# Kernel tuning notes

Measured on AMD Instinct MI355X. Metric: run time of the kernel, lower is better.

Reference implementation:

```python
import jax, jax.numpy as jnp
import numpy as np

N_FIELDS = 8
N_NODES = 100000
N_EDGES = 6400000


def setup_inputs() -> dict:
    key = jax.random.key(0)
    k1, k2, k3, k4, k5 = jax.random.split(key, 5)
    q = jax.random.normal(k1, (N_FIELDS, N_NODES), dtype=jnp.float32)
    edges = jax.random.normal(k2, (N_EDGES, 1), dtype=jnp.float32)
    senders = jax.random.randint(k3, (N_EDGES,), 0, N_NODES, dtype=jnp.int32)
    receivers = jax.random.randint(k4, (N_EDGES,), 0, N_NODES, dtype=jnp.int32)
    dt = jax.random.uniform(k5, (1,), dtype=jnp.float32)
    # learned parameters, initialized exactly as in DeltaQGNN.__init__
    w_self = jnp.linspace(0.05, 0.09, N_FIELDS)
    w_msg = jnp.linspace(0.02, 0.04, N_FIELDS)
    w_edge = jnp.linspace(0.01, 0.03, N_FIELDS)
    b = jnp.linspace(0.005, 0.008, N_FIELDS)
    return {"q": q, "edges": edges, "senders": senders, "receivers": receivers,
            "dt": dt, "w_self": w_self, "w_msg": w_msg, "w_edge": w_edge, "b": b}


def reference(q, edges, senders, receivers, dt, w_self, w_msg, w_edge, b):
    # q: [F, N], edges: [E, 1], senders/receivers: [E], dt: [1]
    n_nodes = q.shape[1]
    edge_scalar = edges[:, 0]                                    # [E]
    # gather sender values for all fields at once: [F, E]
    msg_in = q[:, senders] + w_edge[:, None] * edge_scalar[None, :]
    # scatter-add to receivers per field: [F, N]
    msg = jax.vmap(lambda m: jax.ops.segment_sum(m, receivers, num_segments=n_nodes))(msg_in)
    rhs = w_self[:, None] * q + w_msg[:, None] * msg + b[:, None]
    return dt * rhs                                              # [F, N]
```

## Files before the change

### kernel.cpp

```cpp
#include <hip/hip_runtime.h>

#define NF 8
#define BSHIFT 8
#define BNODES 256
#define MAXNB 512
#define NBLK 512
#define TPBW 1024
#define TPB 256
#define TPR 512
#define CHUNK 4096
#define SPLIT 8
#define CAP 24
#define IDXSTR 26
#define LSLICE 2560

__global__ void k_transpose(const float* __restrict__ q, float* __restrict__ qT,
                            float* __restrict__ govf, int n_nodes) {
    int n = blockIdx.x * blockDim.x + threadIdx.x;
    if (n >= n_nodes) return;
    float4 a, b;
    a.x = q[0 * n_nodes + n]; a.y = q[1 * n_nodes + n];
    a.z = q[2 * n_nodes + n]; a.w = q[3 * n_nodes + n];
    b.x = q[4 * n_nodes + n]; b.y = q[5 * n_nodes + n];
    b.z = q[6 * n_nodes + n]; b.w = q[7 * n_nodes + n];
    float4* dst = reinterpret_cast<float4*>(qT + (size_t)n * NF);
    dst[0] = a; dst[1] = b;
    float* o = govf + (size_t)n * 9;
#pragma unroll
    for (int k = 0; k < 9; ++k) o[k] = 0.f;
}

__global__ __launch_bounds__(TPBW) void k_hist(const int* __restrict__ receivers, int n_edges,
                                               int nb, int tiles, unsigned* __restrict__ cnt) {
    __shared__ unsigned hist[MAXNB];
    for (int t = blockIdx.x; t < tiles; t += gridDim.x) {
        for (int i = threadIdx.x; i < nb; i += blockDim.x) hist[i] = 0;
        __syncthreads();
        int start = t * CHUNK;
        int end = min(start + CHUNK, n_edges);
        for (int e = start + threadIdx.x; e < end; e += blockDim.x)
            atomicAdd(&hist[receivers[e] >> BSHIFT], 1u);
        __syncthreads();
        for (int i = threadIdx.x; i < nb; i += blockDim.x)
            cnt[(size_t)t * nb + i] = hist[i];
        __syncthreads();
    }
}

__global__ void k_scan1(const unsigned* __restrict__ cnt, unsigned* __restrict__ rel,
                        int nb, int tiles, unsigned* __restrict__ tot) {
    int wave = (blockIdx.x * blockDim.x + threadIdx.x) >> 6;
    int lane = threadIdx.x & 63;
    if (wave >= nb) return;
    unsigned carry = 0;
    for (int base = 0; base < tiles; base += 64) {
        int t = base + lane;
        unsigned v = (t < tiles) ? cnt[(size_t)t * nb + wave] : 0u;
        unsigned x = v;
        for (int d = 1; d < 64; d <<= 1) {
            unsigned y = __shfl_up(x, d, 64);
            if (lane >= d) x += y;
        }
        if (t < tiles) rel[(size_t)t * nb + wave] = carry + x - v;
        carry += __shfl(x, 63, 64);
    }
    if (lane == 0) tot[wave] = carry;
}

__global__ void k_scan2(const unsigned* __restrict__ tot, int nb,
                        unsigned* __restrict__ bucket_base) {
    __shared__ unsigned a[MAXNB];
    __shared__ unsigned b[MAXNB];
    int t = threadIdx.x;
    unsigned* src = a;
    unsigned* dst = b;
    if (t < nb) src[t] = tot[t];
    __syncthreads();
    for (int d = 1; d < nb; d <<= 1) {
        if (t < nb) dst[t] = (t >= d) ? src[t] + src[t - d] : src[t];
        __syncthreads();
        unsigned* tmp = src; src = dst; dst = tmp;
    }
    if (t < nb) bucket_base[t + 1] = src[t];
    if (t == 0) bucket_base[0] = 0;
}

__global__ __launch_bounds__(TPBW) void k_scatter(
        const float* __restrict__ edges, const int* __restrict__ senders,
        const int* __restrict__ receivers, int n_edges, int nb, int tiles,
        const unsigned* __restrict__ cnt, const unsigned* __restrict__ rel,
        const unsigned* __restrict__ bucket_base, uint2* __restrict__ rec) {
    __shared__ uint2 lrec[CHUNK];
    __shared__ unsigned short lbkt[CHUNK];
    __shared__ unsigned gbase[MAXNB];
    __shared__ unsigned lbase[MAXNB + 1];
    __shared__ unsigned lcur[MAXNB];

    for (int t = blockIdx.x; t < tiles; t += gridDim.x) {
        for (int bi = threadIdx.x; bi < nb; bi += blockDim.x) {
            gbase[bi] = bucket_base[bi] + rel[(size_t)t * nb + bi];
            lcur[bi] = 0;
        }
        __syncthreads();
        if (threadIdx.x < 64) {
            int lane = threadIdx.x;
            unsigned carry = 0;
            for (int base = 0; base < nb; base += 64) {
                int bi = base + lane;
                unsigned v = (bi < nb) ? cnt[(size_t)t * nb + bi] : 0u;
                unsigned x = v;
                for (int d = 1; d < 64; d <<= 1) {
                    unsigned y = __shfl_up(x, d, 64);
                    if (lane >= d) x += y;
                }
                if (bi < nb) lbase[bi] = carry + x - v;
                carry += __shfl(x, 63, 64);
            }
            if (lane == 0) lbase[nb] = carry;
        }
        __syncthreads();

        int start = t * CHUNK;
        int n = min(CHUNK, n_edges - start);

        for (int i = threadIdx.x; i < n; i += blockDim.x) {
            int e = start + i;
            int s = senders[e];
            int r = receivers[e];
            float ev = edges[e];
            int bkt = r >> BSHIFT;
            unsigned p = atomicAdd(&lcur[bkt], 1u);
            unsigned slot = lbase[bkt] + p;
            uint2 rc;
            rc.x = ((unsigned)(r & (BNODES - 1)) << 17) | (unsigned)s;
            rc.y = __float_as_uint(ev);
            lrec[slot] = rc;
            lbkt[slot] = (unsigned short)bkt;
        }
        __syncthreads();

        for (int j = threadIdx.x; j < n; j += blockDim.x) {
            unsigned bkt = lbkt[j];
            unsigned gaddr = gbase[bkt] + ((unsigned)j - lbase[bkt]);
            rec[gaddr] = lrec[j];
        }
        __syncthreads();
    }
}

__global__ __launch_bounds__(TPR) void k_reduce_slot(
        const uint2* __restrict__ rec, const unsigned* __restrict__ bucket_base,
        const float* __restrict__ qT, float* __restrict__ part,
        float* __restrict__ govf, int n_nodes) {
    __shared__ uint2 lrec[LSLICE];
    __shared__ unsigned short idx[BNODES * IDXSTR];
    __shared__ unsigned cur[BNODES];
    int t = threadIdx.x;
    if (t < BNODES) cur[t] = 0;
    __syncthreads();

    int bkt = blockIdx.x / SPLIT;
    int s   = blockIdx.x % SPLIT;
    unsigned e0 = bucket_base[bkt], e1 = bucket_base[bkt + 1];
    unsigned len = e1 - e0;
    unsigned a0 = e0 + (unsigned)(((unsigned long long)len * s) / SPLIT);
    unsigned a1 = e0 + (unsigned)(((unsigned long long)len * (s + 1)) / SPLIT);
    unsigned slice = a1 - a0;

    for (unsigned i = t; i < slice; i += TPR) {
        uint2 rc = rec[a0 + i];
        if (i < LSLICE) lrec[i] = rc;
        unsigned rl = rc.x >> 17;
        unsigned pos = atomicAdd(&cur[rl], 1u);
        if (pos < CAP) {
            idx[rl * IDXSTR + pos] = (unsigned short)i;
        } else {
            unsigned snd = rc.x & 0x1FFFFu;
            float ev = __uint_as_float(rc.y);
            const float4* qs = reinterpret_cast<const float4*>(qT + (size_t)snd * NF);
            float4 q0 = qs[0];
            float4 q1 = qs[1];
            unsigned node = (unsigned)bkt * BNODES + rl;
            float* a = govf + (size_t)node * 9;
            atomicAdd(a + 0, q0.x); atomicAdd(a + 1, q0.y);
            atomicAdd(a + 2, q0.z); atomicAdd(a + 3, q0.w);
            atomicAdd(a + 4, q1.x); atomicAdd(a + 5, q1.y);
            atomicAdd(a + 6, q1.z); atomicAdd(a + 7, q1.w);
            atomicAdd(a + 8, ev);
        }
    }
    __syncthreads();

    int node = t >> 1;
    int parity = t & 1;
    float m[9];
#pragma unroll
    for (int k = 0; k < 9; ++k) m[k] = 0.f;
    unsigned cntv = cur[node];
    if (cntv > CAP) cntv = CAP;
    for (unsigned j = parity; j < cntv; j += 2) {
        unsigned i0 = idx[node * IDXSTR + j];
        uint2 rc0 = (i0 < LSLICE) ? lrec[i0] : rec[a0 + i0];
        const float4* qs0 = reinterpret_cast<const float4*>(qT + (size_t)(rc0.x & 0x1FFFFu) * NF);
        float4 a0v = qs0[0], a1v = qs0[1];
        m[0] += a0v.x; m[1] += a0v.y; m[2] += a0v.z; m[3] += a0v.w;
        m[4] += a1v.x; m[5] += a1v.y; m[6] += a1v.z; m[7] += a1v.w;
        m[8] += __uint_as_float(rc0.y);
    }
    __syncthreads();

    float* scratch = reinterpret_cast<float*>(lrec);
    if (parity == 1) {
        float* d = scratch + (size_t)node * 9;
#pragma unroll
        for (int k = 0; k < 9; ++k) d[k] = m[k];
    }
    __syncthreads();
    if (parity == 0) {
        const float* p2 = scratch + (size_t)node * 9;
        float* dst = part + (size_t)blockIdx.x * (BNODES * 9) + (size_t)node * 9;
#pragma unroll
        for (int k = 0; k < 9; ++k) dst[k] = m[k] + p2[k];
    }
}

__global__ void k_finalize2(const float* __restrict__ part, const float* __restrict__ govf,
                            const float* __restrict__ q,
                            const float* __restrict__ dtp, const float* __restrict__ w_self,
                            const float* __restrict__ w_msg, const float* __restrict__ w_edge,
                            const float* __restrict__ bv, float* __restrict__ out,
                            int split, int n_nodes) {
    int n = blockIdx.x * blockDim.x + threadIdx.x;
    if (n >= n_nodes) return;
    int bkt = n >> BSHIFT;
    int rl = n & (BNODES - 1);
    float m[9];
#pragma unroll
    for (int f = 0; f < 9; ++f) m[f] = govf[(size_t)n * 9 + f];
    for (int s = 0; s < split; ++s) {
        const float* p = part + ((size_t)(bkt * split + s) * BNODES + rl) * 9;
#pragma unroll
        for (int f = 0; f < 9; ++f) m[f] += p[f];
    }
    float dtv = dtp[0];
    float evs = m[8];
#pragma unroll
    for (int f = 0; f < NF; ++f) {
        float msg = m[f] + w_edge[f] * evs;
        out[(size_t)f * n_nodes + n] =
            dtv * (w_self[f] * q[(size_t)f * n_nodes + n] + w_msg[f] * msg + bv[f]);
    }
}

__global__ void k_reduce_fused(const uint2* __restrict__ rec,
                               const unsigned* __restrict__ bucket_base,
                               const float* __restrict__ qT, const float* __restrict__ q,
                               const float* __restrict__ dtp, const float* __restrict__ w_self,
                               const float* __restrict__ w_msg, const float* __restrict__ w_edge,
                               const float* __restrict__ bv, float* __restrict__ out,
                               int n_nodes) {
    __shared__ float acc[BNODES * 9];
    for (int i = threadIdx.x; i < BNODES * 9; i += blockDim.x) acc[i] = 0.f;
    __syncthreads();
    int bkt = blockIdx.x;
    unsigned e0 = bucket_base[bkt], e1 = bucket_base[bkt + 1];
    for (unsigned e = e0 + threadIdx.x; e < e1; e += blockDim.x) {
        uint2 rc = rec[e];
        unsigned snd = rc.x & 0x1FFFFu;
        unsigned rl = rc.x >> 17;
        float ev = __uint_as_float(rc.y);
        const float4* qs = reinterpret_cast<const float4*>(qT + (size_t)snd * NF);
        float4 q0 = qs[0];
        float4 q1 = qs[1];
        float* a = &acc[rl * 9];
        atomicAdd(a + 0, q0.x); atomicAdd(a + 1, q0.y);
        atomicAdd(a + 2, q0.z); atomicAdd(a + 3, q0.w);
        atomicAdd(a + 4, q1.x); atomicAdd(a + 5, q1.y);
        atomicAdd(a + 6, q1.z); atomicAdd(a + 7, q1.w);
        atomicAdd(a + 8, ev);
    }
    __syncthreads();
    int n = bkt * BNODES + threadIdx.x;
    if (n < n_nodes) {
        float dtv = dtp[0];
        float evs = acc[threadIdx.x * 9 + 8];
#pragma unroll
        for (int f = 0; f < NF; ++f) {
            float msg = acc[threadIdx.x * 9 + f] + w_edge[f] * evs;
            out[(size_t)f * n_nodes + n] =
                dtv * (w_self[f] * q[(size_t)f * n_nodes + n] + w_msg[f] * msg + bv[f]);
        }
    }
}

__global__ void k_transpose_zero(const float* __restrict__ q, float* __restrict__ qT,
                                 float* __restrict__ msgT, int n_nodes) {
    int n = blockIdx.x * blockDim.x + threadIdx.x;
    if (n >= n_nodes) return;
    float v[NF];
#pragma unroll
    for (int f = 0; f < NF; ++f) v[f] = q[f * n_nodes + n];
    float4* dst = reinterpret_cast<float4*>(qT + (size_t)n * NF);
    dst[0] = make_float4(v[0], v[1], v[2], v[3]);
    dst[1] = make_float4(v[4], v[5], v[6], v[7]);
    float4 z = make_float4(0.f, 0.f, 0.f, 0.f);
    float4* m = reinterpret_cast<float4*>(msgT + (size_t)n * NF);
    m[0] = z; m[1] = z;
}

__global__ void k_edge_scatter(const float* __restrict__ edges, const int* __restrict__ senders,
                               const int* __restrict__ receivers, const float* __restrict__ qT,
                               float* __restrict__ msgT, const float* __restrict__ w_edge,
                               int n_edges) {
    float we[NF];
#pragma unroll
    for (int f = 0; f < NF; ++f) we[f] = w_edge[f];
    int idx = blockIdx.x * blockDim.x + threadIdx.x;
    int stride = gridDim.x * blockDim.x;
    for (int e = idx; e < n_edges; e += stride) {
        int s = senders[e];
        int r = receivers[e];
        float ev = edges[e];
        const float4* qs = reinterpret_cast<const float4*>(qT + (size_t)s * NF);
        float4 q0 = qs[0];
        float4 q1 = qs[1];
        float* m = msgT + (size_t)r * NF;
        atomicAdd(m + 0, q0.x + we[0] * ev);
        atomicAdd(m + 1, q0.y + we[1] * ev);
        atomicAdd(m + 2, q0.z + we[2] * ev);
        atomicAdd(m + 3, q0.w + we[3] * ev);
        atomicAdd(m + 4, q1.x + we[4] * ev);
        atomicAdd(m + 5, q1.y + we[5] * ev);
        atomicAdd(m + 6, q1.z + we[6] * ev);
        atomicAdd(m + 7, q1.w + we[7] * ev);
    }
}

__global__ void k_finalize(const float* __restrict__ q, const float* __restrict__ msgT,
                           const float* __restrict__ dt, const float* __restrict__ w_self,
                           const float* __restrict__ w_msg, const float* __restrict__ b,
                           float* __restrict__ out, int n_nodes) {
    int n = blockIdx.x * blockDim.x + threadIdx.x;
    if (n >= n_nodes) return;
    float dtv = dt[0];
    const float4* m4 = reinterpret_cast<const float4*>(msgT + (size_t)n * NF);
    float4 m0 = m4[0];
    float4 m1 = m4[1];
    float mv[NF] = {m0.x, m0.y, m0.z, m0.w, m1.x, m1.y, m1.z, m1.w};
#pragma unroll
    for (int f = 0; f < NF; ++f) {
        out[f * n_nodes + n] = dtv * (w_self[f] * q[f * n_nodes + n] + w_msg[f] * mv[f] + b[f]);
    }
}

extern "C" void kernel_launch(void* const* d_in, const int* in_sizes, int n_in,
                              void* d_out, int out_size, void* d_ws, size_t ws_size,
                              hipStream_t stream) {
    const float* q         = (const float*)d_in[0];
    const float* edges     = (const float*)d_in[1];
    const int*   senders   = (const int*)d_in[2];
    const int*   receivers = (const int*)d_in[3];
    const float* dt        = (const float*)d_in[4];
    const float* w_self    = (const float*)d_in[5];
    const float* w_msg     = (const float*)d_in[6];
    const float* w_edge    = (const float*)d_in[7];
    const float* b         = (const float*)d_in[8];
    float* out = (float*)d_out;

    const int n_nodes = in_sizes[0] / NF;
    const int n_edges = in_sizes[2];
    const int nb = (n_nodes + BNODES - 1) >> BSHIFT;
    const int tiles = (n_edges + CHUNK - 1) / CHUNK;

    size_t rec_bytes   = (size_t)n_edges * 8;
    size_t qT_bytes    = (size_t)n_nodes * NF * 4;
    size_t cnt_bytes   = (size_t)nb * tiles * 4;
    size_t tot_bytes   = (size_t)nb * 4;
    size_t bbase_bytes = (size_t)(nb + 1) * 4;
    size_t govf_bytes  = (size_t)nb * BNODES * 9 * 4;
    size_t fixed = rec_bytes + qT_bytes + 2 * cnt_bytes + tot_bytes + bbase_bytes
                 + govf_bytes + 1024;
    size_t part_bytes = (size_t)SPLIT * nb * BNODES * 9 * 4;

    bool sorted_ok = (n_nodes <= 131072) && (nb <= MAXNB) && (fixed <= ws_size);
    bool slot_ok = sorted_ok && (fixed + part_bytes <= ws_size);

    if (slot_ok) {
        char* p = (char*)d_ws;
        uint2*    rec         = (uint2*)p;    p += rec_bytes;
        float*    qT          = (float*)p;    p += qT_bytes;
        unsigned* cnt         = (unsigned*)p; p += cnt_bytes;
        unsigned* rel         = (unsigned*)p; p += cnt_bytes;
        unsigned* tot         = (unsigned*)p; p += tot_bytes;
        unsigned* bucket_base = (unsigned*)p; p += bbase_bytes;
        float*    govf        = (float*)p;    p += govf_bytes;
        float*    part        = (float*)(((uintptr_t)p + 255) & ~(uintptr_t)255);

        k_transpose<<<(n_nodes + TPB - 1) / TPB, TPB, 0, stream>>>(q, qT, govf, n_nodes);
        k_hist<<<NBLK, TPBW, 0, stream>>>(receivers, n_edges, nb, tiles, cnt);
        k_scan1<<<(nb + 3) / 4, TPB, 0, stream>>>(cnt, rel, nb, tiles, tot);
        k_scan2<<<1, 512, 0, stream>>>(tot, nb, bucket_base);
        k_scatter<<<NBLK, TPBW, 0, stream>>>(edges, senders, receivers, n_edges, nb, tiles,
                                             cnt, rel, bucket_base, rec);
        k_reduce_slot<<<nb * SPLIT, TPR, 0, stream>>>(rec, bucket_base, qT, part,
                                                      govf, n_nodes);
        k_finalize2<<<(n_nodes + TPB - 1) / TPB, TPB, 0, stream>>>(
            part, govf, q, dt, w_self, w_msg, w_edge, b, out, SPLIT, n_nodes);
    } else if (sorted_ok) {
        char* p = (char*)d_ws;
        uint2*    rec         = (uint2*)p;    p += rec_bytes;
        float*    qT          = (float*)p;    p += qT_bytes;
        unsigned* cnt         = (unsigned*)p; p += cnt_bytes;
        unsigned* rel         = (unsigned*)p; p += cnt_bytes;
        unsigned* tot         = (unsigned*)p; p += tot_bytes;
        unsigned* bucket_base = (unsigned*)p; p += bbase_bytes;
        float*    govf        = (float*)p;

        k_transpose<<<(n_nodes + TPB - 1) / TPB, TPB, 0, stream>>>(q, qT, govf, n_nodes);
        k_hist<<<NBLK, TPBW, 0, stream>>>(receivers, n_edges, nb, tiles, cnt);
        k_scan1<<<(nb + 3) / 4, TPB, 0, stream>>>(cnt, rel, nb, tiles, tot);
        k_scan2<<<1, 512, 0, stream>>>(tot, nb, bucket_base);
        k_scatter<<<NBLK, TPBW, 0, stream>>>(edges, senders, receivers, n_edges, nb, tiles,
                                             cnt, rel, bucket_base, rec);
        k_reduce_fused<<<nb, BNODES, 0, stream>>>(rec, bucket_base, qT, q, dt, w_self,
                                                  w_msg, w_edge, b, out, n_nodes);
    } else {
        float* qT   = (float*)d_ws;
        float* msgT = qT + (size_t)n_nodes * NF;
        k_transpose_zero<<<(n_nodes + TPB - 1) / TPB, TPB, 0, stream>>>(q, qT, msgT, n_nodes);
        k_edge_scatter<<<3072, TPB, 0, stream>>>(edges, senders, receivers, qT, msgT,
                                                 w_edge, n_edges);
        k_finalize<<<(n_nodes + TPB - 1) / TPB, TPB, 0, stream>>>(q, msgT, dt, w_self, w_msg,
                                                                  b, out, n_nodes);
    }
}
```

Baseline: 133.4 us.

## Replace per-node capped index lists with LDS counting-sort of edge records

The reduce kernel previously built a fixed-capacity (24) per-node index list in LDS and sent overflow edges to global float atomics. It now counts the first LSLICE records per local node, prefix-scans the counts, and scatters the records into LDS sorted by node, so each node's edges are contiguous and uncapped. Only records beyond LSLICE still go through global atomics. This removes the indirection and most atomic overflow traffic, at the cost of an extra scan step, a barrier, and more registers for the KPT held records.

```diff
diff --git a/kernel.cpp b/kernel.cpp
--- a/kernel.cpp
+++ b/kernel.cpp
@@ -10,9 +10,8 @@
 #define TPR 512
 #define CHUNK 4096
 #define SPLIT 8
-#define CAP 24
-#define IDXSTR 26
 #define LSLICE 2560
+#define KPT 5
 
 __global__ void k_transpose(const float* __restrict__ q, float* __restrict__ qT,
                             float* __restrict__ govf, int n_nodes) {
@@ -152,9 +151,9 @@
         const uint2* __restrict__ rec, const unsigned* __restrict__ bucket_base,
         const float* __restrict__ qT, float* __restrict__ part,
         float* __restrict__ govf, int n_nodes) {
-    __shared__ uint2 lrec[LSLICE];
-    __shared__ unsigned short idx[BNODES * IDXSTR];
+    __shared__ uint2 srec[LSLICE];
     __shared__ unsigned cur[BNODES];
+    __shared__ unsigned nbase[BNODES];
     int t = threadIdx.x;
     if (t < BNODES) cur[t] = 0;
     __syncthreads();
@@ -166,50 +165,79 @@
     unsigned a0 = e0 + (unsigned)(((unsigned long long)len * s) / SPLIT);
     unsigned a1 = e0 + (unsigned)(((unsigned long long)len * (s + 1)) / SPLIT);
     unsigned slice = a1 - a0;
-
-    for (unsigned i = t; i < slice; i += TPR) {
+    unsigned lds_n = slice < LSLICE ? slice : LSLICE;
+
+    uint2    r0[KPT];
+    unsigned p0[KPT];
+#pragma unroll
+    for (int k = 0; k < KPT; ++k) {
+        unsigned i = (unsigned)t + (unsigned)k * TPR;
+        p0[k] = 0xFFFFFFFFu;
+        if (i < lds_n) {
+            uint2 rc = rec[a0 + i];
+            r0[k] = rc;
+            p0[k] = atomicAdd(&cur[rc.x >> 17], 1u);
+        }
+    }
+    for (unsigned i = LSLICE + t; i < slice; i += TPR) {
         uint2 rc = rec[a0 + i];
-        if (i < LSLICE) lrec[i] = rc;
+        unsigned snd = rc.x & 0x1FFFFu;
         unsigned rl = rc.x >> 17;
-        unsigned pos = atomicAdd(&cur[rl], 1u);
-        if (pos < CAP) {
-            idx[rl * IDXSTR + pos] = (unsigned short)i;
-        } else {
-            unsigned snd = rc.x & 0x1FFFFu;
-            float ev = __uint_as_float(rc.y);
-            const float4* qs = reinterpret_cast<const float4*>(qT + (size_t)snd * NF);
-            float4 q0 = qs[0];
-            float4 q1 = qs[1];
-            unsigned node = (unsigned)bkt * BNODES + rl;
-            float* a = govf + (size_t)node * 9;
-            atomicAdd(a + 0, q0.x); atomicAdd(a + 1, q0.y);
-            atomicAdd(a + 2, q0.z); atomicAdd(a + 3, q0.w);
-            atomicAdd(a + 4, q1.x); atomicAdd(a + 5, q1.y);
-            atomicAdd(a + 6, q1.z); atomicAdd(a + 7, q1.w);
-            atomicAdd(a + 8, ev);
+        float ev = __uint_as_float(rc.y);
+        const float4* qs = reinterpret_cast<const float4*>(qT + (size_t)snd * NF);
+        float4 q0 = qs[0];
+        float4 q1 = qs[1];
+        float* a = govf + ((size_t)bkt * BNODES + rl) * 9;
+        atomicAdd(a + 0, q0.x); atomicAdd(a + 1, q0.y);
+        atomicAdd(a + 2, q0.z); atomicAdd(a + 3, q0.w);
+        atomicAdd(a + 4, q1.x); atomicAdd(a + 5, q1.y);
+        atomicAdd(a + 6, q1.z); atomicAdd(a + 7, q1.w);
+        atomicAdd(a + 8, ev);
+    }
+    __syncthreads();
+
+    if (t < 64) {
+        unsigned carry = 0;
+        for (int c = 0; c < BNODES; c += 64) {
+            unsigned v = cur[c + t];
+            unsigned x = v;
+            for (int d = 1; d < 64; d <<= 1) {
+                unsigned y = __shfl_up(x, d, 64);
+                if (t >= d) x += y;
+            }
+            nbase[c + t] = carry + x - v;
+            carry += __shfl(x, 63, 64);
+        }
+    }
+    __syncthreads();
+
+#pragma unroll
+    for (int k = 0; k < KPT; ++k) {
+        if (p0[k] != 0xFFFFFFFFu) {
+            unsigned rl = r0[k].x >> 17;
+            srec[nbase[rl] + p0[k]] = r0[k];
         }
     }
     __syncthreads();
 
     int node = t >> 1;
     int parity = t & 1;
+    unsigned nb0 = nbase[node];
+    unsigned ncnt = cur[node];
     float m[9];
 #pragma unroll
     for (int k = 0; k < 9; ++k) m[k] = 0.f;
-    unsigned cntv = cur[node];
-    if (cntv > CAP) cntv = CAP;
-    for (unsigned j = parity; j < cntv; j += 2) {
-        unsigned i0 = idx[node * IDXSTR + j];
-        uint2 rc0 = (i0 < LSLICE) ? lrec[i0] : rec[a0 + i0];
-        const float4* qs0 = reinterpret_cast<const float4*>(qT + (size_t)(rc0.x & 0x1FFFFu) * NF);
-        float4 a0v = qs0[0], a1v = qs0[1];
+    for (unsigned j = parity; j < ncnt; j += 2) {
+        uint2 rc = srec[nb0 + j];
+        const float4* qs = reinterpret_cast<const float4*>(qT + (size_t)(rc.x & 0x1FFFFu) * NF);
+        float4 a0v = qs[0], a1v = qs[1];
         m[0] += a0v.x; m[1] += a0v.y; m[2] += a0v.z; m[3] += a0v.w;
         m[4] += a1v.x; m[5] += a1v.y; m[6] += a1v.z; m[7] += a1v.w;
-        m[8] += __uint_as_float(rc0.y);
-    }
-    __syncthreads();
-
-    float* scratch = reinterpret_cast<float*>(lrec);
+        m[8] += __uint_as_float(rc.y);
+    }
+    __syncthreads();
+
+    float* scratch = reinterpret_cast<float*>(srec);
     if (parity == 1) {
         float* d = scratch + (size_t)node * 9;
 #pragma unroll
```

New measurement: 135.2 us. No clear change (+1.4%).

## Replace histogram/scan bucket sort with fixed-capacity buckets and atomic cursors

Applied to the files above, without the earlier changes.

Drops the separate histogram, two scan kernels and tiled scatter. A single fused scatter kernel now builds a per-chunk local histogram and reserves space in fixed-capacity per-bucket regions through global atomic cursors. Edges that overflow a bucket's capacity are accumulated directly with global float atomics. This removes three kernel launches and a full extra pass over receivers, at the cost of padded bucket storage and an overflow path whose cost depends on how evenly receivers are distributed across buckets.

```diff
diff --git a/kernel.cpp b/kernel.cpp
--- a/kernel.cpp
+++ b/kernel.cpp
@@ -4,19 +4,21 @@
 #define BSHIFT 8
 #define BNODES 256
 #define MAXNB 512
-#define NBLK 512
-#define TPBW 1024
 #define TPB 256
 #define TPR 512
-#define CHUNK 4096
+#define TPBF 1024
+#define CHUNKF 12288
+#define CAPB 17408
 #define SPLIT 8
 #define CAP 24
 #define IDXSTR 26
 #define LSLICE 2560
 
 __global__ void k_transpose(const float* __restrict__ q, float* __restrict__ qT,
-                            float* __restrict__ govf, int n_nodes) {
+                            float* __restrict__ govf, unsigned* __restrict__ gcur,
+                            int n_nodes, int nb) {
     int n = blockIdx.x * blockDim.x + threadIdx.x;
+    if (n < nb) gcur[n] = 0u;
     if (n >= n_nodes) return;
     float4 a, b;
     a.x = q[0 * n_nodes + n]; a.y = q[1 * n_nodes + n];
@@ -30,126 +32,90 @@
     for (int k = 0; k < 9; ++k) o[k] = 0.f;
 }
 
-__global__ __launch_bounds__(TPBW) void k_hist(const int* __restrict__ receivers, int n_edges,
-                                               int nb, int tiles, unsigned* __restrict__ cnt) {
+__global__ __launch_bounds__(TPBF) void k_scatter_fused(
+        const float* __restrict__ edges, const int* __restrict__ senders,
+        const int* __restrict__ receivers, int n_edges, int nb,
+        unsigned* __restrict__ gcur, const float* __restrict__ qT,
+        float* __restrict__ govf, uint2* __restrict__ rec) {
+    __shared__ uint2 lrec[CHUNKF];
+    __shared__ unsigned short lbkt[CHUNKF];
     __shared__ unsigned hist[MAXNB];
-    for (int t = blockIdx.x; t < tiles; t += gridDim.x) {
-        for (int i = threadIdx.x; i < nb; i += blockDim.x) hist[i] = 0;
-        __syncthreads();
-        int start = t * CHUNK;
-        int end = min(start + CHUNK, n_edges);
-        for (int e = start + threadIdx.x; e < end; e += blockDim.x)
-            atomicAdd(&hist[receivers[e] >> BSHIFT], 1u);
-        __syncthreads();
-        for (int i = threadIdx.x; i < nb; i += blockDim.x)
-            cnt[(size_t)t * nb + i] = hist[i];
-        __syncthreads();
-    }
-}
-
-__global__ void k_scan1(const unsigned* __restrict__ cnt, unsigned* __restrict__ rel,
-                        int nb, int tiles, unsigned* __restrict__ tot) {
-    int wave = (blockIdx.x * blockDim.x + threadIdx.x) >> 6;
-    int lane = threadIdx.x & 63;
-    if (wave >= nb) return;
-    unsigned carry = 0;
-    for (int base = 0; base < tiles; base += 64) {
-        int t = base + lane;
-        unsigned v = (t < tiles) ? cnt[(size_t)t * nb + wave] : 0u;
-        unsigned x = v;
-        for (int d = 1; d < 64; d <<= 1) {
-            unsigned y = __shfl_up(x, d, 64);
-            if (lane >= d) x += y;
+    __shared__ unsigned lbase[MAXNB];
+    __shared__ unsigned gbase[MAXNB];
+    __shared__ unsigned lcur[MAXNB];
+
+    int start = blockIdx.x * CHUNKF;
+    int end = min(start + CHUNKF, n_edges);
+    int n = end - start;
+    if (n <= 0) return;
+
+    for (int i = threadIdx.x; i < nb; i += TPBF) { hist[i] = 0u; lcur[i] = 0u; }
+    __syncthreads();
+
+    for (int i = threadIdx.x; i < n; i += TPBF)
+        atomicAdd(&hist[receivers[start + i] >> BSHIFT], 1u);
+    __syncthreads();
+
+    if (threadIdx.x < (unsigned)nb)
+        gbase[threadIdx.x] = atomicAdd(&gcur[threadIdx.x], hist[threadIdx.x]);
+    if (threadIdx.x < 64) {
+        int lane = threadIdx.x;
+        unsigned carry = 0;
+        for (int base = 0; base < nb; base += 64) {
+            int bi = base + lane;
+            unsigned v = (bi < nb) ? hist[bi] : 0u;
+            unsigned x = v;
+            for (int d = 1; d < 64; d <<= 1) {
+                unsigned y = __shfl_up(x, d, 64);
+                if (lane >= d) x += y;
+            }
+            if (bi < nb) lbase[bi] = carry + x - v;
+            carry += __shfl(x, 63, 64);
         }
-        if (t < tiles) rel[(size_t)t * nb + wave] = carry + x - v;
-        carry += __shfl(x, 63, 64);
-    }
-    if (lane == 0) tot[wave] = carry;
-}
-
-__global__ void k_scan2(const unsigned* __restrict__ tot, int nb,
-                        unsigned* __restrict__ bucket_base) {
-    __shared__ unsigned a[MAXNB];
-    __shared__ unsigned b[MAXNB];
-    int t = threadIdx.x;
-    unsigned* src = a;
-    unsigned* dst = b;
-    if (t < nb) src[t] = tot[t];
-    __syncthreads();
-    for (int d = 1; d < nb; d <<= 1) {
-        if (t < nb) dst[t] = (t >= d) ? src[t] + src[t - d] : src[t];
-        __syncthreads();
-        unsigned* tmp = src; src = dst; dst = tmp;
-    }
-    if (t < nb) bucket_base[t + 1] = src[t];
-    if (t == 0) bucket_base[0] = 0;
-}
-
-__global__ __launch_bounds__(TPBW) void k_scatter(
-        const float* __restrict__ edges, const int* __restrict__ senders,
-        const int* __restrict__ receivers, int n_edges, int nb, int tiles,
-        const unsigned* __restrict__ cnt, const unsigned* __restrict__ rel,
-        const unsigned* __restrict__ bucket_base, uint2* __restrict__ rec) {
-    __shared__ uint2 lrec[CHUNK];
-    __shared__ unsigned short lbkt[CHUNK];
-    __shared__ unsigned gbase[MAXNB];
-    __shared__ unsigned lbase[MAXNB + 1];
-    __shared__ unsigned lcur[MAXNB];
-
-    for (int t = blockIdx.x; t < tiles; t += gridDim.x) {
-        for (int bi = threadIdx.x; bi < nb; bi += blockDim.x) {
-            gbase[bi] = bucket_base[bi] + rel[(size_t)t * nb + bi];
-            lcur[bi] = 0;
+    }
+    __syncthreads();
+
+    for (int i = threadIdx.x; i < n; i += TPBF) {
+        int e = start + i;
+        int s = senders[e];
+        int r = receivers[e];
+        float ev = edges[e];
+        int bkt = r >> BSHIFT;
+        unsigned p = atomicAdd(&lcur[bkt], 1u);
+        unsigned slot = lbase[bkt] + p;
+        uint2 rc;
+        rc.x = ((unsigned)(r & (BNODES - 1)) << 17) | (unsigned)s;
+        rc.y = __float_as_uint(ev);
+        lrec[slot] = rc;
+        lbkt[slot] = (unsigned short)bkt;
+    }
+    __syncthreads();
+
+    for (int j = threadIdx.x; j < n; j += TPBF) {
+        unsigned bkt = lbkt[j];
+        uint2 rc = lrec[j];
+        unsigned off = gbase[bkt] + ((unsigned)j - lbase[bkt]);
+        if (off < CAPB) {
+            rec[(size_t)bkt * CAPB + off] = rc;
+        } else {
+            unsigned snd = rc.x & 0x1FFFFu;
+            unsigned rl = rc.x >> 17;
+            float ev = __uint_as_float(rc.y);
+            const float4* qs = reinterpret_cast<const float4*>(qT + (size_t)snd * NF);
+            float4 q0 = qs[0];
+            float4 q1 = qs[1];
+            float* a = govf + ((size_t)bkt * BNODES + rl) * 9;
+            atomicAdd(a + 0, q0.x); atomicAdd(a + 1, q0.y);
+            atomicAdd(a + 2, q0.z); atomicAdd(a + 3, q0.w);
+            atomicAdd(a + 4, q1.x); atomicAdd(a + 5, q1.y);
+            atomicAdd(a + 6, q1.z); atomicAdd(a + 7, q1.w);
+            atomicAdd(a + 8, ev);
         }
-        __syncthreads();
-        if (threadIdx.x < 64) {
-            int lane = threadIdx.x;
-            unsigned carry = 0;
-            for (int base = 0; base < nb; base += 64) {
-                int bi = base + lane;
-                unsigned v = (bi < nb) ? cnt[(size_t)t * nb + bi] : 0u;
-                unsigned x = v;
-                for (int d = 1; d < 64; d <<= 1) {
-                    unsigned y = __shfl_up(x, d, 64);
-                    if (lane >= d) x += y;
-                }
-                if (bi < nb) lbase[bi] = carry + x - v;
-                carry += __shfl(x, 63, 64);
-            }
-            if (lane == 0) lbase[nb] = carry;
-        }
-        __syncthreads();
-
-        int start = t * CHUNK;
-        int n = min(CHUNK, n_edges - start);
-
-        for (int i = threadIdx.x; i < n; i += blockDim.x) {
-            int e = start + i;
-            int s = senders[e];
-            int r = receivers[e];
-            float ev = edges[e];
-            int bkt = r >> BSHIFT;
-            unsigned p = atomicAdd(&lcur[bkt], 1u);
-            unsigned slot = lbase[bkt] + p;
-            uint2 rc;
-            rc.x = ((unsigned)(r & (BNODES - 1)) << 17) | (unsigned)s;
-            rc.y = __float_as_uint(ev);
-            lrec[slot] = rc;
-            lbkt[slot] = (unsigned short)bkt;
-        }
-        __syncthreads();
-
-        for (int j = threadIdx.x; j < n; j += blockDim.x) {
-            unsigned bkt = lbkt[j];
-            unsigned gaddr = gbase[bkt] + ((unsigned)j - lbase[bkt]);
-            rec[gaddr] = lrec[j];
-        }
-        __syncthreads();
     }
 }
 
 __global__ __launch_bounds__(TPR) void k_reduce_slot(
-        const uint2* __restrict__ rec, const unsigned* __restrict__ bucket_base,
+        const uint2* __restrict__ rec, const unsigned* __restrict__ gcur,
         const float* __restrict__ qT, float* __restrict__ part,
         float* __restrict__ govf, int n_nodes) {
     __shared__ uint2 lrec[LSLICE];
@@ -161,14 +127,15 @@
 
     int bkt = blockIdx.x / SPLIT;
     int s   = blockIdx.x % SPLIT;
-    unsigned e0 = bucket_base[bkt], e1 = bucket_base[bkt + 1];
-    unsigned len = e1 - e0;
-    unsigned a0 = e0 + (unsigned)(((unsigned long long)len * s) / SPLIT);
-    unsigned a1 = e0 + (unsigned)(((unsigned long long)len * (s + 1)) / SPLIT);
+    unsigned len = gcur[bkt];
+    if (len > CAPB) len = CAPB;
+    size_t base = (size_t)bkt * CAPB;
+    unsigned a0 = (unsigned)(((unsigned long long)len * s) / SPLIT);
+    unsigned a1 = (unsigned)(((unsigned long long)len * (s + 1)) / SPLIT);
     unsigned slice = a1 - a0;
 
     for (unsigned i = t; i < slice; i += TPR) {
-        uint2 rc = rec[a0 + i];
+        uint2 rc = rec[base + a0 + i];
         if (i < LSLICE) lrec[i] = rc;
         unsigned rl = rc.x >> 17;
         unsigned pos = atomicAdd(&cur[rl], 1u);
@@ -180,8 +147,7 @@
             const float4* qs = reinterpret_cast<const float4*>(qT + (size_t)snd * NF);
             float4 q0 = qs[0];
             float4 q1 = qs[1];
-            unsigned node = (unsigned)bkt * BNODES + rl;
-            float* a = govf + (size_t)node * 9;
+            float* a = govf + ((size_t)bkt * BNODES + rl) * 9;
             atomicAdd(a + 0, q0.x); atomicAdd(a + 1, q0.y);
             atomicAdd(a + 2, q0.z); atomicAdd(a + 3, q0.w);
             atomicAdd(a + 4, q1.x); atomicAdd(a + 5, q1.y);
@@ -200,7 +166,7 @@
     if (cntv > CAP) cntv = CAP;
     for (unsigned j = parity; j < cntv; j += 2) {
         unsigned i0 = idx[node * IDXSTR + j];
-        uint2 rc0 = (i0 < LSLICE) ? lrec[i0] : rec[a0 + i0];
+        uint2 rc0 = (i0 < LSLICE) ? lrec[i0] : rec[base + a0 + i0];
         const float4* qs0 = reinterpret_cast<const float4*>(qT + (size_t)(rc0.x & 0x1FFFFu) * NF);
         float4 a0v = qs0[0], a1v = qs0[1];
         m[0] += a0v.x; m[1] += a0v.y; m[2] += a0v.z; m[3] += a0v.w;
@@ -249,47 +215,6 @@
         float msg = m[f] + w_edge[f] * evs;
         out[(size_t)f * n_nodes + n] =
             dtv * (w_self[f] * q[(size_t)f * n_nodes + n] + w_msg[f] * msg + bv[f]);
-    }
-}
-
-__global__ void k_reduce_fused(const uint2* __restrict__ rec,
-                               const unsigned* __restrict__ bucket_base,
-                               const float* __restrict__ qT, const float* __restrict__ q,
-                               const float* __restrict__ dtp, const float* __restrict__ w_self,
-                               const float* __restrict__ w_msg, const float* __restrict__ w_edge,
-                               const float* __restrict__ bv, float* __restrict__ out,
-                               int n_nodes) {
-    __shared__ float acc[BNODES * 9];
-    for (int i = threadIdx.x; i < BNODES * 9; i += blockDim.x) acc[i] = 0.f;
-    __syncthreads();
-    int bkt = blockIdx.x;
-    unsigned e0 = bucket_base[bkt], e1 = bucket_base[bkt + 1];
-    for (unsigned e = e0 + threadIdx.x; e < e1; e += blockDim.x) {
-        uint2 rc = rec[e];
-        unsigned snd = rc.x & 0x1FFFFu;
-        unsigned rl = rc.x >> 17;
-        float ev = __uint_as_float(rc.y);
-        const float4* qs = reinterpret_cast<const float4*>(qT + (size_t)snd * NF);
-        float4 q0 = qs[0];
-        float4 q1 = qs[1];
-        float* a = &acc[rl * 9];
-        atomicAdd(a + 0, q0.x); atomicAdd(a + 1, q0.y);
-        atomicAdd(a + 2, q0.z); atomicAdd(a + 3, q0.w);
-        atomicAdd(a + 4, q1.x); atomicAdd(a + 5, q1.y);
-        atomicAdd(a + 6, q1.z); atomicAdd(a + 7, q1.w);
-        atomicAdd(a + 8, ev);
-    }
-    __syncthreads();
-    int n = bkt * BNODES + threadIdx.x;
-    if (n < n_nodes) {
-        float dtv = dtp[0];
-        float evs = acc[threadIdx.x * 9 + 8];
-#pragma unroll
-        for (int f = 0; f < NF; ++f) {
-            float msg = acc[threadIdx.x * 9 + f] + w_edge[f] * evs;
-            out[(size_t)f * n_nodes + n] =
-                dtv * (w_self[f] * q[(size_t)f * n_nodes + n] + w_msg[f] * msg + bv[f]);
-        }
     }
 }
 
@@ -370,60 +295,35 @@
     const int n_nodes = in_sizes[0] / NF;
     const int n_edges = in_sizes[2];
     const int nb = (n_nodes + BNODES - 1) >> BSHIFT;
-    const int tiles = (n_edges + CHUNK - 1) / CHUNK;
-
-    size_t rec_bytes   = (size_t)n_edges * 8;
-    size_t qT_bytes    = (size_t)n_nodes * NF * 4;
-    size_t cnt_bytes   = (size_t)nb * tiles * 4;
-    size_t tot_bytes   = (size_t)nb * 4;
-    size_t bbase_bytes = (size_t)(nb + 1) * 4;
-    size_t govf_bytes  = (size_t)nb * BNODES * 9 * 4;
-    size_t fixed = rec_bytes + qT_bytes + 2 * cnt_bytes + tot_bytes + bbase_bytes
-                 + govf_bytes + 1024;
+
+    size_t rec_bytes  = (size_t)nb * CAPB * 8;
+    size_t qT_bytes   = (size_t)n_nodes * NF * 4;
+    size_t gcur_bytes = 256 + (size_t)nb * 4;
+    size_t govf_bytes = (size_t)nb * BNODES * 9 * 4;
     size_t part_bytes = (size_t)SPLIT * nb * BNODES * 9 * 4;
-
-    bool sorted_ok = (n_nodes <= 131072) && (nb <= MAXNB) && (fixed <= ws_size);
-    bool slot_ok = sorted_ok && (fixed + part_bytes <= ws_size);
-
-    if (slot_ok) {
+    size_t need = rec_bytes + qT_bytes + gcur_bytes + govf_bytes + part_bytes + 1024;
+
+    double mean_per_bucket = (double)n_edges / (double)nb;
+    bool ok = (n_nodes <= 131072) && (nb <= MAXNB) && (need <= ws_size) &&
+              (mean_per_bucket + 8.0 * __builtin_sqrt(mean_per_bucket) < (double)CAPB);
+
+    if (ok) {
         char* p = (char*)d_ws;
-        uint2*    rec         = (uint2*)p;    p += rec_bytes;
-        float*    qT          = (float*)p;    p += qT_bytes;
-        unsigned* cnt         = (unsigned*)p; p += cnt_bytes;
-        unsigned* rel         = (unsigned*)p; p += cnt_bytes;
-        unsigned* tot         = (unsigned*)p; p += tot_bytes;
-        unsigned* bucket_base = (unsigned*)p; p += bbase_bytes;
-        float*    govf        = (float*)p;    p += govf_bytes;
-        float*    part        = (float*)(((uintptr_t)p + 255) & ~(uintptr_t)255);
-
-        k_transpose<<<(n_nodes + TPB - 1) / TPB, TPB, 0, stream>>>(q, qT, govf, n_nodes);
-        k_hist<<<NBLK, TPBW, 0, stream>>>(receivers, n_edges, nb, tiles, cnt);
-        k_scan1<<<(nb + 3) / 4, TPB, 0, stream>>>(cnt, rel, nb, tiles, tot);
-        k_scan2<<<1, 512, 0, stream>>>(tot, nb, bucket_base);
-        k_scatter<<<NBLK, TPBW, 0, stream>>>(edges, senders, receivers, n_edges, nb, tiles,
-                                             cnt, rel, bucket_base, rec);
-        k_reduce_slot<<<nb * SPLIT, TPR, 0, stream>>>(rec, bucket_base, qT, part,
-                                                      govf, n_nodes);
+        uint2*    rec  = (uint2*)p;    p += rec_bytes;
+        float*    qT   = (float*)p;    p += qT_bytes;
+        unsigned* gcur = (unsigned*)p; p += gcur_bytes;
+        float*    govf = (float*)p;    p += govf_bytes;
+        float*    part = (float*)(((uintptr_t)p + 255) & ~(uintptr_t)255);
+
+        int nblk_f = (n_edges + CHUNKF - 1) / CHUNKF;
+
+        k_transpose<<<(n_nodes + TPB - 1) / TPB, TPB, 0, stream>>>(q, qT, govf, gcur,
+                                                                   n_nodes, nb);
+        k_scatter_fused<<<nblk_f, TPBF, 0, stream>>>(edges, senders, receivers, n_edges,
+                                                     nb, gcur, qT, govf, rec);
+        k_reduce_slot<<<nb * SPLIT, TPR, 0, stream>>>(rec, gcur, qT, part, govf, n_nodes);
         k_finalize2<<<(n_nodes + TPB - 1) / TPB, TPB, 0, stream>>>(
             part, govf, q, dt, w_self, w_msg, w_edge, b, out, SPLIT, n_nodes);
-    } else if (sorted_ok) {
-        char* p = (char*)d_ws;
-        uint2*    rec         = (uint2*)p;    p += rec_bytes;
-        float*    qT          = (float*)p;    p += qT_bytes;
-        unsigned* cnt         = (unsigned*)p; p += cnt_bytes;
-        unsigned* rel         = (unsigned*)p; p += cnt_bytes;
-        unsigned* tot         = (unsigned*)p; p += tot_bytes;
-        unsigned* bucket_base = (unsigned*)p; p += bbase_bytes;
-        float*    govf        = (float*)p;
-
-        k_transpose<<<(n_nodes + TPB - 1) / TPB, TPB, 0, stream>>>(q, qT, govf, n_nodes);
-        k_hist<<<NBLK, TPBW, 0, stream>>>(receivers, n_edges, nb, tiles, cnt);
-        k_scan1<<<(nb + 3) / 4, TPB, 0, stream>>>(cnt, rel, nb, tiles, tot);
-        k_scan2<<<1, 512, 0, stream>>>(tot, nb, bucket_base);
-        k_scatter<<<NBLK, TPBW, 0, stream>>>(edges, senders, receivers, n_edges, nb, tiles,
-                                             cnt, rel, bucket_base, rec);
-        k_reduce_fused<<<nb, BNODES, 0, stream>>>(rec, bucket_base, qT, q, dt, w_self,
-                                                  w_msg, w_edge, b, out, n_nodes);
     } else {
         float* qT   = (float*)d_ws;
         float* msgT = qT + (size_t)n_nodes * NF;
```

After: 111.3 us. 1.2x faster.
